# Kernel optimization log

Hardware: AMD Instinct MI355X
Metric: run time of the kernel (lower is better)

Reference implementation:

```python
import jax, jax.numpy as jnp
import numpy as np

B, N, C, H = 16, 577, 384, 6
ONE_DIM = 24
RPD = 2 * ONE_DIM - 1  # 47
NUM_CLS = 1
HEAD_DIM = C // H
SCALE = HEAD_DIM ** -0.5


def _build_rel_pos_index():
    # Faithful to the torch loop: tmp[dy - y + off, dx - x + off] with
    # torch's negative-index wraparound -> modulo RPD.
    off = ONE_DIM // 2
    qy = np.repeat(np.arange(ONE_DIM), ONE_DIM)  # (Np,) y of each query patch
    qx = np.tile(np.arange(ONE_DIM), ONE_DIM)    # (Np,) x of each query patch
    ky, kx = qy, qx                              # key patches use same grid
    ry = (ky[None, :] - qy[:, None] + off) % RPD
    rx = (kx[None, :] - qx[:, None] + off) % RPD
    return jnp.asarray(ry * RPD + rx, dtype=jnp.int32)  # (Np, Np)


def setup_inputs() -> dict:
    key = jax.random.key(0)
    k = jax.random.split(key, 6)
    x = jax.random.normal(k[0], (B, N, C), dtype=jnp.float32)
    qkv_w = jax.random.normal(k[1], (3 * C, C), dtype=jnp.float32) * 0.02
    qkv_b = jnp.zeros((3 * C,), dtype=jnp.float32)
    proj_w = jax.random.normal(k[2], (C, C), dtype=jnp.float32) * 0.02
    proj_b = jnp.zeros((C,), dtype=jnp.float32)
    rel_pos = jax.random.normal(k[3], (H, RPD * RPD), dtype=jnp.float32) * 0.02
    mask = jax.random.randint(k[4], (B, N, N), 0, 2, dtype=jnp.int32)
    return {
        "x": x, "qkv_w": qkv_w, "qkv_b": qkv_b,
        "proj_w": proj_w, "proj_b": proj_b, "rel_pos": rel_pos,
        "rel_pos_index": _build_rel_pos_index(),
        "mask": mask, "patch_attn": 1,
    }


def reference(x, qkv_w, qkv_b, proj_w, proj_b, rel_pos, rel_pos_index, mask, patch_attn):
    # qkv projection: torch Linear -> x @ W^T + b
    qkv = x @ qkv_w.T + qkv_b                               # (B, N, 3C)
    qkv = qkv.reshape(B, N, 3, H, HEAD_DIM).transpose(2, 0, 3, 1, 4)
    q, k, v = qkv[0], qkv[1], qkv[2]                        # (B, H, N, hd)

    attn = jnp.einsum("bhqd,bhkd->bhqk", q, k) * SCALE      # (B, H, N, N)

    if patch_attn:
        # gather per-head relative-position bias for patch tokens
        bias = rel_pos[:, rel_pos_index]                    # (H, Np, Np)
        attn = attn.at[:, :, NUM_CLS:, NUM_CLS:].add(bias)

    neg = jnp.finfo(attn.dtype).min
    attn = jnp.where(mask[:, None, :, :] == 0, neg, attn)   # broadcast over heads

    attn = jax.nn.softmax(attn, axis=-1)
    out = jnp.einsum("bhqk,bhkd->bhqd", attn, v)            # (B, H, N, hd)
    out = out.transpose(0, 2, 1, 3).reshape(B, N, C)
    out = out @ proj_w.T + proj_b
    return out
```

## Files before the change

### kernel.cpp

```cpp
#include <hip/hip_runtime.h>
#include <float.h>
#include <math.h>

#define NB 16
#define NN 577
#define NC 384
#define NH 6
#define ND 64
#define RPD2 2209
#define MTOT 9232
#define MPAD 9344
#define SCALE_ 0.125f
#define NEGBIG -3.0e38f
#define BSTRIDE 580
#define NKPAD 640

typedef __attribute__((ext_vector_type(8))) short bf16x8;
typedef __attribute__((ext_vector_type(4))) float f32x4;
typedef unsigned short u16;

#define MFMA16(a, b, c) __builtin_amdgcn_mfma_f32_16x16x32_bf16(a, b, c, 0, 0, 0)

#define SQA 3932160ull
#define OFF_QH 0ull
#define OFF_QL SQA
#define OFF_KH (2ull * SQA)
#define OFF_KL (3ull * SQA)
#define OFF_VTH (4ull * SQA)
#define OFF_VTL (5ull * SQA)
#define OFF_XH (6ull * SQA)
#define OFF_XL (6ull * SQA + 3588096ull)
#define OFF_WQH (6ull * SQA + 2ull * 3588096ull)
#define OFF_WQL (OFF_WQH + 442368ull)
#define OFF_WPH (OFF_WQL + 442368ull)
#define OFF_WPL (OFF_WPH + 147456ull)
#define OFF_BT  (OFF_WPL + 147456ull)
#define OFF_PM  (OFF_BT + 2007960ull)

static __device__ __forceinline__ u16 f2bf(float f) {
  unsigned u = __float_as_uint(f);
  u += 0x7fff + ((u >> 16) & 1);
  return (u16)(u >> 16);
}
static __device__ __forceinline__ float bf2f(u16 h) {
  return __uint_as_float((unsigned)h << 16);
}
static __device__ __forceinline__ void split2(float v, u16& hi, u16& lo) {
  hi = f2bf(v);
  lo = f2bf(v - bf2f(hi));
}
static __device__ __forceinline__ void gload16(const void* g, void* l) {
  __builtin_amdgcn_global_load_lds(
      (const __attribute__((address_space(1))) void*)g,
      (__attribute__((address_space(3))) void*)l, 16, 0, 0);
}

__global__ __launch_bounds__(256) void split_inputs_k(
    const float* __restrict__ x, const float* __restrict__ wq,
    const float* __restrict__ wp, u16* __restrict__ ws)
{
  const int q = blockIdx.x * 256 + threadIdx.x;
  float4 v = {0.f, 0.f, 0.f, 0.f};
  u16 *dh, *dl;
  if (q < 897024) {
    if (q < 886272) v = ((const float4*)x)[q];
    dh = ws + OFF_XH + 4ull * q;
    dl = ws + OFF_XL + 4ull * q;
  } else if (q < 1007616) {
    int t = q - 897024;
    v = ((const float4*)wq)[t];
    dh = ws + OFF_WQH + 4ull * t;
    dl = ws + OFF_WQL + 4ull * t;
  } else {
    int t = q - 1007616;
    v = ((const float4*)wp)[t];
    dh = ws + OFF_WPH + 4ull * t;
    dl = ws + OFF_WPL + 4ull * t;
  }
  ushort4 hh, ll;
  split2(v.x, hh.x, ll.x);
  split2(v.y, hh.y, ll.y);
  split2(v.z, hh.z, ll.z);
  split2(v.w, hh.w, ll.w);
  *(ushort4*)dh = hh;
  *(ushort4*)dl = ll;
}

__global__ __launch_bounds__(256) void pack_mask_k(const int* __restrict__ mask,
                                                   unsigned* __restrict__ pm)
{
  const int wid = (blockIdx.x * 256 + threadIdx.x) >> 6;
  const int lane = threadIdx.x & 63;
  if (wid >= MTOT) return;
  const int* mr = mask + (size_t)wid * NN;
#pragma unroll
  for (int c = 0; c < 10; ++c) {
    int k = c * 64 + lane;
    int v = (k < NN) ? mr[k] : 0;
    unsigned long long bal = __ballot(v != 0);
    if (lane == 0) pm[wid * 20 + 2 * c] = (unsigned)bal;
    if (lane == 1) pm[wid * 20 + 2 * c + 1] = (unsigned)(bal >> 32);
  }
}

__global__ __launch_bounds__(256) void bias_build_k(
    const float* __restrict__ rel_pos, const int* __restrict__ rel_idx,
    const int* __restrict__ patch, u16* __restrict__ tbl)
{
  const int q = blockIdx.x;
  const int h = blockIdx.y;
  const int pa = *patch;
  u16* row = tbl + ((size_t)h * NN + q) * BSTRIDE;
  for (int kk = threadIdx.x; kk < BSTRIDE; kk += 256) {
    float v = 0.f;
    if (pa && q >= 1 && kk >= 1 && kk < NN)
      v = rel_pos[h * RPD2 + rel_idx[(q - 1) * 576 + (kk - 1)]];
    row[kk] = f2bf(v);
  }
}

__global__ __launch_bounds__(256, 3) void qkv_mfma_k(
    const u16* __restrict__ Xh, const u16* __restrict__ Xl,
    const u16* __restrict__ Wh, const u16* __restrict__ Wl,
    const float* __restrict__ bias, u16* __restrict__ ws)
{
  __shared__ u16 Ash[4096], Asl[4096];
  __shared__ u16 Bsh[4096], Bsl[4096];

  const int tid = threadIdx.x;
  const int w = tid >> 6, l = tid & 63, lq = l & 15, lg = l >> 4;
  const int wm = (w >> 1) * 64, wn = (w & 1) * 64;
  const int mb = blockIdx.x * 128;
  const int rb = blockIdx.y * 128;
  const int r0 = rb + wn;
  const int soff = (l >> 2) * 384 + (l & 3) * 8;

  f32x4 acc[4][4];
#pragma unroll
  for (int nt = 0; nt < 4; ++nt) {
    float bv = bias[r0 + 16 * nt + lq];
#pragma unroll
    for (int mt = 0; mt < 4; ++mt) acc[mt][nt] = (f32x4){bv, bv, bv, bv};
  }

  for (int k0 = 0; k0 < 384; k0 += 32) {
    __syncthreads();
#pragma unroll
    for (int j = 0; j < 2; ++j) {
      const int tr = 32 * w + 16 * j;
      const size_t ga = (size_t)(mb + tr) * 384 + k0 + soff;
      const size_t gb = (size_t)(rb + tr) * 384 + k0 + soff;
      gload16(&Xh[ga], &Ash[tr * 32]);
      gload16(&Xl[ga], &Asl[tr * 32]);
      gload16(&Wh[gb], &Bsh[tr * 32]);
      gload16(&Wl[gb], &Bsl[tr * 32]);
    }
    __syncthreads();

    bf16x8 bhf[4], blf[4];
#pragma unroll
    for (int nt = 0; nt < 4; ++nt) {
      bhf[nt] = *(const bf16x8*)&Bsh[(wn + 16 * nt + lq) * 32 + 8 * lg];
      blf[nt] = *(const bf16x8*)&Bsl[(wn + 16 * nt + lq) * 32 + 8 * lg];
    }
#pragma unroll
    for (int mt = 0; mt < 4; ++mt) {
      bf16x8 ah = *(const bf16x8*)&Ash[(wm + 16 * mt + lq) * 32 + 8 * lg];
      bf16x8 al = *(const bf16x8*)&Asl[(wm + 16 * mt + lq) * 32 + 8 * lg];
#pragma unroll
      for (int nt = 0; nt < 4; ++nt) {
        acc[mt][nt] = MFMA16(ah, bhf[nt], acc[mt][nt]);
        acc[mt][nt] = MFMA16(ah, blf[nt], acc[mt][nt]);
        acc[mt][nt] = MFMA16(al, bhf[nt], acc[mt][nt]);
      }
    }
  }

  const int comp = rb / 384;
  const int h = ((rb % 384) + wn) >> 6;
#pragma unroll
  for (int mt = 0; mt < 4; ++mt)
#pragma unroll
    for (int r = 0; r < 4; ++r) {
      int m = mb + wm + 16 * mt + 4 * lg + r;
      if (m >= MTOT) continue;
      int bb = m / NN, nn = m - bb * NN;
      int bh = bb * NH + h;
#pragma unroll
      for (int nt = 0; nt < 4; ++nt) {
        int d = 16 * nt + lq;
        float v = acc[mt][nt][r];
        u16 hi, lo;
        if (comp == 0) {
          v *= SCALE_;
          split2(v, hi, lo);
          size_t a = ((size_t)bh * NKPAD + nn) * 64 + d;
          ws[OFF_QH + a] = hi;
          ws[OFF_QL + a] = lo;
        } else if (comp == 1) {
          split2(v, hi, lo);
          size_t a = ((size_t)bh * NKPAD + nn) * 64 + d;
          ws[OFF_KH + a] = hi;
          ws[OFF_KL + a] = lo;
        } else {
          split2(v, hi, lo);
          size_t a = ((size_t)bh * 64 + d) * NKPAD + nn;
          ws[OFF_VTH + a] = hi;
          ws[OFF_VTL + a] = lo;
        }
      }
    }
}

__global__ __launch_bounds__(256, 2) void attn_k(
    const u16* __restrict__ Qh, const u16* __restrict__ Ql,
    const u16* __restrict__ Kh, const u16* __restrict__ Kl,
    const u16* __restrict__ Vth, const u16* __restrict__ Vtl,
    const u16* __restrict__ btbl, const unsigned* __restrict__ pm,
    u16* __restrict__ Oh, u16* __restrict__ Ol)
{
  __shared__ u16 Kth[2][4096], Ktl[2][4096];
  __shared__ u16 Vsh[2][4096], Vsl[2][4096];
  __shared__ u16 Ph[4][1024];

  const int tid = threadIdx.x;
  const int w = tid >> 6, l = tid & 63, lq = l & 15, lg = l >> 4;
  const int q0 = blockIdx.x * 64;
  const int h = blockIdx.y, b = blockIdx.z;
  const int bh = b * NH + h;
  const int qrow = q0 + 16 * w + lq;
  const int swz = (lq & 7) << 3;
  const int ln8 = l >> 3, lc8 = l & 7;
  const int koff = ln8 * 64 + ((lc8 ^ ln8) << 3);
  const int voff = ln8 * NKPAD + ((lc8 ^ ln8) << 3);

#define STAGE(ch, bf)                                                        \
  {                                                                          \
    const int kb_ = (ch) * 64;                                               \
    const size_t kgb = ((size_t)bh * NKPAD + kb_ + 16 * w) * 64 + koff;      \
    const size_t vgb = ((size_t)bh * 64 + 16 * w) * NKPAD + kb_ + voff;      \
    gload16(&Kh[kgb],              &Kth[bf][(16 * w) * 64]);                 \
    gload16(&Kh[kgb + 512],        &Kth[bf][(16 * w + 8) * 64]);             \
    gload16(&Kl[kgb],              &Ktl[bf][(16 * w) * 64]);                 \
    gload16(&Kl[kgb + 512],        &Ktl[bf][(16 * w + 8) * 64]);             \
    gload16(&Vth[vgb],             &Vsh[bf][(16 * w) * 64]);                 \
    gload16(&Vth[vgb + 8 * NKPAD], &Vsh[bf][(16 * w + 8) * 64]);             \
    gload16(&Vtl[vgb],             &Vsl[bf][(16 * w) * 64]);                 \
    gload16(&Vtl[vgb + 8 * NKPAD], &Vsl[bf][(16 * w + 8) * 64]);             \
  }

  STAGE(0, 0);

  const size_t qbase = ((size_t)bh * NKPAD + qrow) * 64 + 8 * lg;
  bf16x8 qbh[2], qbl[2];
  qbh[0] = *(const bf16x8*)&Qh[qbase];
  qbh[1] = *(const bf16x8*)&Qh[qbase + 32];
  qbl[0] = *(const bf16x8*)&Ql[qbase];
  qbl[1] = *(const bf16x8*)&Ql[qbase + 32];

  const bool qv = qrow < NN;
  const int gqc = qv ? qrow : NN - 1;
  const unsigned* pmrow = pm + ((size_t)b * NN + gqc) * 20;
  const size_t brow = ((size_t)h * NN + gqc) * BSTRIDE;

  float m_reg = NEGBIG, l_reg = 0.f;
  f32x4 accO[4] = {};

  for (int ch = 0; ch < 10; ++ch) {
    const int kb = ch * 64;
    const int bf = ch & 1;
    __syncthreads();
    if (ch < 9) STAGE(ch + 1, bf ^ 1);

    unsigned long long m64 = (unsigned long long)pmrow[2 * ch] |
                             ((unsigned long long)pmrow[2 * ch + 1] << 32);
    f32x4 cinit[4];
#pragma unroll
    for (int t = 0; t < 4; ++t) {
      cinit[t] = (f32x4){0.f, 0.f, 0.f, 0.f};
      int kkb = kb + 16 * t + 4 * lg;
      if (qv && kkb <= 576) {
        ushort4 b4 = *(const ushort4*)&btbl[brow + kkb];
        cinit[t][0] = bf2f(b4.x); cinit[t][1] = bf2f(b4.y);
        cinit[t][2] = bf2f(b4.z); cinit[t][3] = bf2f(b4.w);
      }
    }

    float sv[4][4];
#pragma unroll
    for (int t = 0; t < 4; ++t) {
      f32x4 acc = cinit[t];
      const int ar = (16 * t + lq) * 64;
#pragma unroll
      for (int ks = 0; ks < 2; ++ks) {
        const int c = (8 * lg + 32 * ks) ^ swz;
        bf16x8 ah = *(const bf16x8*)&Kth[bf][ar + c];
        bf16x8 al = *(const bf16x8*)&Ktl[bf][ar + c];
        acc = MFMA16(ah, qbh[ks], acc);
        acc = MFMA16(ah, qbl[ks], acc);
        acc = MFMA16(al, qbh[ks], acc);
      }
      sv[t][0] = acc[0]; sv[t][1] = acc[1];
      sv[t][2] = acc[2]; sv[t][3] = acc[3];
    }

    float cmax = NEGBIG;
#pragma unroll
    for (int t = 0; t < 4; ++t)
#pragma unroll
      for (int r = 0; r < 4; ++r) {
        int kl = 16 * t + 4 * lg + r;
        float s = ((m64 >> kl) & 1ull) ? sv[t][r] : NEGBIG;
        sv[t][r] = s;
        cmax = fmaxf(cmax, s);
      }
    cmax = fmaxf(cmax, __shfl_xor(cmax, 16));
    cmax = fmaxf(cmax, __shfl_xor(cmax, 32));
    float m_new = fmaxf(m_reg, cmax);
    float fx = __expf(m_reg - m_new);
    float csum = 0.f;
    float ev[4][4];
#pragma unroll
    for (int t = 0; t < 4; ++t)
#pragma unroll
      for (int r = 0; r < 4; ++r) {
        float e = __expf(sv[t][r] - m_new);
        ev[t][r] = e;
        csum += e;
      }
    csum += __shfl_xor(csum, 16);
    csum += __shfl_xor(csum, 32);
    l_reg = l_reg * fx + csum;
    m_reg = m_new;

#pragma unroll
    for (int t = 0; t < 4; ++t) {
      ushort4 ph;
      ph.x = f2bf(ev[t][0]);
      ph.y = f2bf(ev[t][1]);
      ph.z = f2bf(ev[t][2]);
      ph.w = f2bf(ev[t][3]);
      int c = (16 * t + 4 * lg) ^ swz;
      *(ushort4*)&Ph[w][lq * 64 + c] = ph;
    }

    float fxr[4];
#pragma unroll
    for (int r = 0; r < 4; ++r) fxr[r] = __shfl(fx, 4 * lg + r);
#pragma unroll
    for (int t = 0; t < 4; ++t) {
      accO[t][0] *= fxr[0]; accO[t][1] *= fxr[1];
      accO[t][2] *= fxr[2]; accO[t][3] *= fxr[3];
    }

    bf16x8 pah[2];
#pragma unroll
    for (int ks = 0; ks < 2; ++ks) {
      int c = (8 * lg + 32 * ks) ^ swz;
      pah[ks] = *(const bf16x8*)&Ph[w][lq * 64 + c];
    }

#pragma unroll
    for (int t = 0; t < 4; ++t) {
      const int vr = (16 * t + lq) * 64;
#pragma unroll
      for (int ks = 0; ks < 2; ++ks) {
        const int c = (8 * lg + 32 * ks) ^ swz;
        bf16x8 vh = *(const bf16x8*)&Vsh[bf][vr + c];
        bf16x8 vl = *(const bf16x8*)&Vsl[bf][vr + c];
        accO[t] = MFMA16(pah[ks], vh, accO[t]);
        accO[t] = MFMA16(pah[ks], vl, accO[t]);
      }
    }
  }

  float il = 1.f / l_reg;
  float ilr[4];
#pragma unroll
  for (int r = 0; r < 4; ++r) ilr[r] = __shfl(il, 4 * lg + r);
#pragma unroll
  for (int t = 0; t < 4; ++t)
#pragma unroll
    for (int r = 0; r < 4; ++r) {
      int gq2 = q0 + 16 * w + 4 * lg + r;
      if (gq2 < NN) {
        float v = accO[t][r] * ilr[r];
        u16 hi, lo;
        split2(v, hi, lo);
        size_t a = ((size_t)b * NN + gq2) * NC + h * 64 + 16 * t + lq;
        Oh[a] = hi;
        Ol[a] = lo;
      }
    }
#undef STAGE
}

__global__ __launch_bounds__(256, 3) void proj_mfma_k(
    const u16* __restrict__ Ah, const u16* __restrict__ Al,
    const u16* __restrict__ Wh, const u16* __restrict__ Wl,
    const float* __restrict__ bias, float* __restrict__ out)
{
  __shared__ u16 Ash[4096], Asl[4096];
  __shared__ u16 Bsh[4096], Bsl[4096];

  const int tid = threadIdx.x;
  const int w = tid >> 6, l = tid & 63, lq = l & 15, lg = l >> 4;
  const int wm = (w >> 1) * 64, wn = (w & 1) * 64;
  const int mb = blockIdx.x * 128;
  const int rb = blockIdx.y * 128;
  const int r0 = rb + wn;
  const int soff = (l >> 2) * 384 + (l & 3) * 8;

  f32x4 acc[4][4];
#pragma unroll
  for (int nt = 0; nt < 4; ++nt) {
    float bv = bias[r0 + 16 * nt + lq];
#pragma unroll
    for (int mt = 0; mt < 4; ++mt) acc[mt][nt] = (f32x4){bv, bv, bv, bv};
  }

  for (int k0 = 0; k0 < 384; k0 += 32) {
    __syncthreads();
#pragma unroll
    for (int j = 0; j < 2; ++j) {
      const int tr = 32 * w + 16 * j;
      const size_t ga = (size_t)(mb + tr) * 384 + k0 + soff;
      const size_t gb = (size_t)(rb + tr) * 384 + k0 + soff;
      gload16(&Ah[ga], &Ash[tr * 32]);
      gload16(&Al[ga], &Asl[tr * 32]);
      gload16(&Wh[gb], &Bsh[tr * 32]);
      gload16(&Wl[gb], &Bsl[tr * 32]);
    }
    __syncthreads();

    bf16x8 bhf[4], blf[4];
#pragma unroll
    for (int nt = 0; nt < 4; ++nt) {
      bhf[nt] = *(const bf16x8*)&Bsh[(wn + 16 * nt + lq) * 32 + 8 * lg];
      blf[nt] = *(const bf16x8*)&Bsl[(wn + 16 * nt + lq) * 32 + 8 * lg];
    }
#pragma unroll
    for (int mt = 0; mt < 4; ++mt) {
      bf16x8 ah = *(const bf16x8*)&Ash[(wm + 16 * mt + lq) * 32 + 8 * lg];
      bf16x8 al = *(const bf16x8*)&Asl[(wm + 16 * mt + lq) * 32 + 8 * lg];
#pragma unroll
      for (int nt = 0; nt < 4; ++nt) {
        acc[mt][nt] = MFMA16(ah, bhf[nt], acc[mt][nt]);
        acc[mt][nt] = MFMA16(ah, blf[nt], acc[mt][nt]);
        acc[mt][nt] = MFMA16(al, bhf[nt], acc[mt][nt]);
      }
    }
  }

#pragma unroll
  for (int mt = 0; mt < 4; ++mt)
#pragma unroll
    for (int r = 0; r < 4; ++r) {
      int m = mb + wm + 16 * mt + 4 * lg + r;
      if (m >= MTOT) continue;
#pragma unroll
      for (int nt = 0; nt < 4; ++nt)
        out[(size_t)m * NC + r0 + 16 * nt + lq] = acc[mt][nt][r];
    }
}

extern "C" void kernel_launch(void* const* d_in, const int* in_sizes, int n_in,
                              void* d_out, int out_size, void* d_ws, size_t ws_size,
                              hipStream_t stream) {
  const float* x       = (const float*)d_in[0];
  const float* qkv_w   = (const float*)d_in[1];
  const float* qkv_b   = (const float*)d_in[2];
  const float* proj_w  = (const float*)d_in[3];
  const float* proj_b  = (const float*)d_in[4];
  const float* rel_pos = (const float*)d_in[5];
  const int*   rel_idx = (const int*)d_in[6];
  const int*   mask    = (const int*)d_in[7];
  const int*   patch   = (const int*)d_in[8];
  float* out = (float*)d_out;
  u16* W16 = (u16*)d_ws;

  unsigned* pmp = (unsigned*)(W16 + OFF_PM);
  u16* btblp = W16 + OFF_BT;

  split_inputs_k<<<4080, 256, 0, stream>>>(x, qkv_w, proj_w, W16);
  pack_mask_k<<<2308, 256, 0, stream>>>(mask, pmp);
  bias_build_k<<<dim3(NN, NH), 256, 0, stream>>>(rel_pos, rel_idx, patch, btblp);
  qkv_mfma_k<<<dim3(73, 9), 256, 0, stream>>>(
      W16 + OFF_XH, W16 + OFF_XL, W16 + OFF_WQH, W16 + OFF_WQL, qkv_b, W16);
  attn_k<<<dim3(10, NH, NB), 256, 0, stream>>>(
      W16 + OFF_QH, W16 + OFF_QL, W16 + OFF_KH, W16 + OFF_KL,
      W16 + OFF_VTH, W16 + OFF_VTL, btblp, pmp,
      W16 + OFF_XH, W16 + OFF_XL);
  proj_mfma_k<<<dim3(73, 3), 256, 0, stream>>>(
      W16 + OFF_XH, W16 + OFF_XL, W16 + OFF_WPH, W16 + OFF_WPL, proj_b, out);
}
```

Measured before the change: 171.2 us.

## Double query tile per attention block; stream weights directly and double-buffer A in GEMMs

The attention kernel now handles 128 query rows per block, with each wave owning two 16-row query tiles. Every staged K/V chunk is therefore reused for twice as many queries, and the grid shrinks from 10 to 5 query blocks per (batch, head). The QKV and projection GEMMs no longer stage weight tiles in shared memory; they read the B fragments straight from global memory and double-buffer the activation tile, which removes one barrier per k-step. In exchange, attention register pressure roughly doubles and the grid gets smaller, and the direct weight loads depend on cache hits.

```diff
diff --git a/kernel.cpp b/kernel.cpp
--- a/kernel.cpp
+++ b/kernel.cpp
@@ -124,8 +124,7 @@
     const u16* __restrict__ Wh, const u16* __restrict__ Wl,
     const float* __restrict__ bias, u16* __restrict__ ws)
 {
-  __shared__ u16 Ash[4096], Asl[4096];
-  __shared__ u16 Bsh[4096], Bsl[4096];
+  __shared__ u16 Ash[2][4096], Asl[2][4096];
 
   const int tid = threadIdx.x;
   const int w = tid >> 6, l = tid & 63, lq = l & 15, lg = l >> 4;
@@ -135,6 +134,19 @@
   const int r0 = rb + wn;
   const int soff = (l >> 2) * 384 + (l & 3) * 8;
 
+#define STAGE_A(k0_, bf_)                                                    \
+  {                                                                          \
+    _Pragma("unroll")                                                        \
+    for (int j = 0; j < 2; ++j) {                                            \
+      const int tr = 32 * w + 16 * j;                                        \
+      const size_t ga = (size_t)(mb + tr) * 384 + (k0_) + soff;              \
+      gload16(&Xh[ga], &Ash[bf_][tr * 32]);                                  \
+      gload16(&Xl[ga], &Asl[bf_][tr * 32]);                                  \
+    }                                                                        \
+  }
+
+  STAGE_A(0, 0);
+
   f32x4 acc[4][4];
 #pragma unroll
   for (int nt = 0; nt < 4; ++nt) {
@@ -143,30 +155,22 @@
     for (int mt = 0; mt < 4; ++mt) acc[mt][nt] = (f32x4){bv, bv, bv, bv};
   }
 
+  const size_t brow = (size_t)(r0 + lq) * 384 + 8 * lg;
   for (int k0 = 0; k0 < 384; k0 += 32) {
+    const int bf = (k0 >> 5) & 1;
     __syncthreads();
-#pragma unroll
-    for (int j = 0; j < 2; ++j) {
-      const int tr = 32 * w + 16 * j;
-      const size_t ga = (size_t)(mb + tr) * 384 + k0 + soff;
-      const size_t gb = (size_t)(rb + tr) * 384 + k0 + soff;
-      gload16(&Xh[ga], &Ash[tr * 32]);
-      gload16(&Xl[ga], &Asl[tr * 32]);
-      gload16(&Wh[gb], &Bsh[tr * 32]);
-      gload16(&Wl[gb], &Bsl[tr * 32]);
-    }
-    __syncthreads();
+    if (k0 < 352) STAGE_A(k0 + 32, bf ^ 1);
 
     bf16x8 bhf[4], blf[4];
 #pragma unroll
     for (int nt = 0; nt < 4; ++nt) {
-      bhf[nt] = *(const bf16x8*)&Bsh[(wn + 16 * nt + lq) * 32 + 8 * lg];
-      blf[nt] = *(const bf16x8*)&Bsl[(wn + 16 * nt + lq) * 32 + 8 * lg];
+      bhf[nt] = *(const bf16x8*)&Wh[brow + (size_t)(16 * nt) * 384 + k0];
+      blf[nt] = *(const bf16x8*)&Wl[brow + (size_t)(16 * nt) * 384 + k0];
     }
 #pragma unroll
     for (int mt = 0; mt < 4; ++mt) {
-      bf16x8 ah = *(const bf16x8*)&Ash[(wm + 16 * mt + lq) * 32 + 8 * lg];
-      bf16x8 al = *(const bf16x8*)&Asl[(wm + 16 * mt + lq) * 32 + 8 * lg];
+      bf16x8 ah = *(const bf16x8*)&Ash[bf][(wm + 16 * mt + lq) * 32 + 8 * lg];
+      bf16x8 al = *(const bf16x8*)&Asl[bf][(wm + 16 * mt + lq) * 32 + 8 * lg];
 #pragma unroll
       for (int nt = 0; nt < 4; ++nt) {
         acc[mt][nt] = MFMA16(ah, bhf[nt], acc[mt][nt]);
@@ -175,6 +179,7 @@
       }
     }
   }
+#undef STAGE_A
 
   const int comp = rb / 384;
   const int h = ((rb % 384) + wn) >> 6;
@@ -221,14 +226,15 @@
 {
   __shared__ u16 Kth[2][4096], Ktl[2][4096];
   __shared__ u16 Vsh[2][4096], Vsl[2][4096];
-  __shared__ u16 Ph[4][1024];
+  __shared__ u16 Ph[4][2048];
 
   const int tid = threadIdx.x;
   const int w = tid >> 6, l = tid & 63, lq = l & 15, lg = l >> 4;
-  const int q0 = blockIdx.x * 64;
+  const int q0 = blockIdx.x * 128;
   const int h = blockIdx.y, b = blockIdx.z;
   const int bh = b * NH + h;
-  const int qrow = q0 + 16 * w + lq;
+  const int qr0 = q0 + 32 * w + lq;
+  const int qr1 = qr0 + 16;
   const int swz = (lq & 7) << 3;
   const int ln8 = l >> 3, lc8 = l & 7;
   const int koff = ln8 * 64 + ((lc8 ^ ln8) << 3);
@@ -251,20 +257,29 @@
 
   STAGE(0, 0);
 
-  const size_t qbase = ((size_t)bh * NKPAD + qrow) * 64 + 8 * lg;
-  bf16x8 qbh[2], qbl[2];
-  qbh[0] = *(const bf16x8*)&Qh[qbase];
-  qbh[1] = *(const bf16x8*)&Qh[qbase + 32];
-  qbl[0] = *(const bf16x8*)&Ql[qbase];
-  qbl[1] = *(const bf16x8*)&Ql[qbase + 32];
-
-  const bool qv = qrow < NN;
-  const int gqc = qv ? qrow : NN - 1;
-  const unsigned* pmrow = pm + ((size_t)b * NN + gqc) * 20;
-  const size_t brow = ((size_t)h * NN + gqc) * BSTRIDE;
-
-  float m_reg = NEGBIG, l_reg = 0.f;
-  f32x4 accO[4] = {};
+  const size_t qb0 = ((size_t)bh * NKPAD + qr0) * 64 + 8 * lg;
+  const size_t qb1 = ((size_t)bh * NKPAD + qr1) * 64 + 8 * lg;
+  bf16x8 q0h[2], q0l[2], q1h[2], q1l[2];
+  q0h[0] = *(const bf16x8*)&Qh[qb0];
+  q0h[1] = *(const bf16x8*)&Qh[qb0 + 32];
+  q0l[0] = *(const bf16x8*)&Ql[qb0];
+  q0l[1] = *(const bf16x8*)&Ql[qb0 + 32];
+  q1h[0] = *(const bf16x8*)&Qh[qb1];
+  q1h[1] = *(const bf16x8*)&Qh[qb1 + 32];
+  q1l[0] = *(const bf16x8*)&Ql[qb1];
+  q1l[1] = *(const bf16x8*)&Ql[qb1 + 32];
+
+  const int gq0 = (qr0 < NN) ? qr0 : NN - 1;
+  const int gq1 = (qr1 < NN) ? qr1 : NN - 1;
+  const bool qv0 = qr0 < NN, qv1 = qr1 < NN;
+  const unsigned* pmrow0 = pm + ((size_t)b * NN + gq0) * 20;
+  const unsigned* pmrow1 = pm + ((size_t)b * NN + gq1) * 20;
+  const size_t brow0 = ((size_t)h * NN + gq0) * BSTRIDE;
+  const size_t brow1 = ((size_t)h * NN + gq1) * BSTRIDE;
+
+  float m_reg0 = NEGBIG, l_reg0 = 0.f;
+  float m_reg1 = NEGBIG, l_reg1 = 0.f;
+  f32x4 accO0[4] = {}, accO1[4] = {};
 
   for (int ch = 0; ch < 10; ++ch) {
     const int kb = ch * 64;
@@ -272,92 +287,138 @@
     __syncthreads();
     if (ch < 9) STAGE(ch + 1, bf ^ 1);
 
-    unsigned long long m64 = (unsigned long long)pmrow[2 * ch] |
-                             ((unsigned long long)pmrow[2 * ch + 1] << 32);
-    f32x4 cinit[4];
+    unsigned long long m64_0 = (unsigned long long)pmrow0[2 * ch] |
+                               ((unsigned long long)pmrow0[2 * ch + 1] << 32);
+    unsigned long long m64_1 = (unsigned long long)pmrow1[2 * ch] |
+                               ((unsigned long long)pmrow1[2 * ch + 1] << 32);
+    f32x4 ci0[4], ci1[4];
 #pragma unroll
     for (int t = 0; t < 4; ++t) {
-      cinit[t] = (f32x4){0.f, 0.f, 0.f, 0.f};
+      ci0[t] = (f32x4){0.f, 0.f, 0.f, 0.f};
+      ci1[t] = (f32x4){0.f, 0.f, 0.f, 0.f};
       int kkb = kb + 16 * t + 4 * lg;
-      if (qv && kkb <= 576) {
-        ushort4 b4 = *(const ushort4*)&btbl[brow + kkb];
-        cinit[t][0] = bf2f(b4.x); cinit[t][1] = bf2f(b4.y);
-        cinit[t][2] = bf2f(b4.z); cinit[t][3] = bf2f(b4.w);
-      }
-    }
-
-    float sv[4][4];
+      if (kkb <= 576) {
+        if (qv0) {
+          ushort4 b4 = *(const ushort4*)&btbl[brow0 + kkb];
+          ci0[t][0] = bf2f(b4.x); ci0[t][1] = bf2f(b4.y);
+          ci0[t][2] = bf2f(b4.z); ci0[t][3] = bf2f(b4.w);
+        }
+        if (qv1) {
+          ushort4 b4 = *(const ushort4*)&btbl[brow1 + kkb];
+          ci1[t][0] = bf2f(b4.x); ci1[t][1] = bf2f(b4.y);
+          ci1[t][2] = bf2f(b4.z); ci1[t][3] = bf2f(b4.w);
+        }
+      }
+    }
+
+    float sv0[4][4], sv1[4][4];
 #pragma unroll
     for (int t = 0; t < 4; ++t) {
-      f32x4 acc = cinit[t];
+      f32x4 a0 = ci0[t], a1 = ci1[t];
       const int ar = (16 * t + lq) * 64;
 #pragma unroll
       for (int ks = 0; ks < 2; ++ks) {
         const int c = (8 * lg + 32 * ks) ^ swz;
         bf16x8 ah = *(const bf16x8*)&Kth[bf][ar + c];
         bf16x8 al = *(const bf16x8*)&Ktl[bf][ar + c];
-        acc = MFMA16(ah, qbh[ks], acc);
-        acc = MFMA16(ah, qbl[ks], acc);
-        acc = MFMA16(al, qbh[ks], acc);
-      }
-      sv[t][0] = acc[0]; sv[t][1] = acc[1];
-      sv[t][2] = acc[2]; sv[t][3] = acc[3];
-    }
-
-    float cmax = NEGBIG;
-#pragma unroll
-    for (int t = 0; t < 4; ++t)
-#pragma unroll
-      for (int r = 0; r < 4; ++r) {
-        int kl = 16 * t + 4 * lg + r;
-        float s = ((m64 >> kl) & 1ull) ? sv[t][r] : NEGBIG;
-        sv[t][r] = s;
-        cmax = fmaxf(cmax, s);
-      }
-    cmax = fmaxf(cmax, __shfl_xor(cmax, 16));
-    cmax = fmaxf(cmax, __shfl_xor(cmax, 32));
-    float m_new = fmaxf(m_reg, cmax);
-    float fx = __expf(m_reg - m_new);
-    float csum = 0.f;
-    float ev[4][4];
-#pragma unroll
-    for (int t = 0; t < 4; ++t)
-#pragma unroll
-      for (int r = 0; r < 4; ++r) {
-        float e = __expf(sv[t][r] - m_new);
-        ev[t][r] = e;
-        csum += e;
-      }
-    csum += __shfl_xor(csum, 16);
-    csum += __shfl_xor(csum, 32);
-    l_reg = l_reg * fx + csum;
-    m_reg = m_new;
-
-#pragma unroll
-    for (int t = 0; t < 4; ++t) {
-      ushort4 ph;
-      ph.x = f2bf(ev[t][0]);
-      ph.y = f2bf(ev[t][1]);
-      ph.z = f2bf(ev[t][2]);
-      ph.w = f2bf(ev[t][3]);
-      int c = (16 * t + 4 * lg) ^ swz;
-      *(ushort4*)&Ph[w][lq * 64 + c] = ph;
-    }
-
-    float fxr[4];
-#pragma unroll
-    for (int r = 0; r < 4; ++r) fxr[r] = __shfl(fx, 4 * lg + r);
-#pragma unroll
-    for (int t = 0; t < 4; ++t) {
-      accO[t][0] *= fxr[0]; accO[t][1] *= fxr[1];
-      accO[t][2] *= fxr[2]; accO[t][3] *= fxr[3];
-    }
-
-    bf16x8 pah[2];
+        a0 = MFMA16(ah, q0h[ks], a0);
+        a0 = MFMA16(ah, q0l[ks], a0);
+        a0 = MFMA16(al, q0h[ks], a0);
+        a1 = MFMA16(ah, q1h[ks], a1);
+        a1 = MFMA16(ah, q1l[ks], a1);
+        a1 = MFMA16(al, q1h[ks], a1);
+      }
+#pragma unroll
+      for (int r = 0; r < 4; ++r) { sv0[t][r] = a0[r]; sv1[t][r] = a1[r]; }
+    }
+
+    {
+      float cmax = NEGBIG;
+#pragma unroll
+      for (int t = 0; t < 4; ++t)
+#pragma unroll
+        for (int r = 0; r < 4; ++r) {
+          int kl = 16 * t + 4 * lg + r;
+          float s = ((m64_0 >> kl) & 1ull) ? sv0[t][r] : NEGBIG;
+          sv0[t][r] = s;
+          cmax = fmaxf(cmax, s);
+        }
+      cmax = fmaxf(cmax, __shfl_xor(cmax, 16));
+      cmax = fmaxf(cmax, __shfl_xor(cmax, 32));
+      float m_new = fmaxf(m_reg0, cmax);
+      float fx = __expf(m_reg0 - m_new);
+      float csum = 0.f;
+#pragma unroll
+      for (int t = 0; t < 4; ++t) {
+        float e0 = __expf(sv0[t][0] - m_new);
+        float e1 = __expf(sv0[t][1] - m_new);
+        float e2 = __expf(sv0[t][2] - m_new);
+        float e3 = __expf(sv0[t][3] - m_new);
+        csum += e0 + e1 + e2 + e3;
+        ushort4 ph;
+        ph.x = f2bf(e0); ph.y = f2bf(e1); ph.z = f2bf(e2); ph.w = f2bf(e3);
+        *(ushort4*)&Ph[w][lq * 64 + ((16 * t + 4 * lg) ^ swz)] = ph;
+      }
+      csum += __shfl_xor(csum, 16);
+      csum += __shfl_xor(csum, 32);
+      l_reg0 = l_reg0 * fx + csum;
+      m_reg0 = m_new;
+      float fxr[4];
+#pragma unroll
+      for (int r = 0; r < 4; ++r) fxr[r] = __shfl(fx, 4 * lg + r);
+#pragma unroll
+      for (int t = 0; t < 4; ++t) {
+        accO0[t][0] *= fxr[0]; accO0[t][1] *= fxr[1];
+        accO0[t][2] *= fxr[2]; accO0[t][3] *= fxr[3];
+      }
+    }
+    {
+      float cmax = NEGBIG;
+#pragma unroll
+      for (int t = 0; t < 4; ++t)
+#pragma unroll
+        for (int r = 0; r < 4; ++r) {
+          int kl = 16 * t + 4 * lg + r;
+          float s = ((m64_1 >> kl) & 1ull) ? sv1[t][r] : NEGBIG;
+          sv1[t][r] = s;
+          cmax = fmaxf(cmax, s);
+        }
+      cmax = fmaxf(cmax, __shfl_xor(cmax, 16));
+      cmax = fmaxf(cmax, __shfl_xor(cmax, 32));
+      float m_new = fmaxf(m_reg1, cmax);
+      float fx = __expf(m_reg1 - m_new);
+      float csum = 0.f;
+#pragma unroll
+      for (int t = 0; t < 4; ++t) {
+        float e0 = __expf(sv1[t][0] - m_new);
+        float e1 = __expf(sv1[t][1] - m_new);
+        float e2 = __expf(sv1[t][2] - m_new);
+        float e3 = __expf(sv1[t][3] - m_new);
+        csum += e0 + e1 + e2 + e3;
+        ushort4 ph;
+        ph.x = f2bf(e0); ph.y = f2bf(e1); ph.z = f2bf(e2); ph.w = f2bf(e3);
+        *(ushort4*)&Ph[w][(16 + lq) * 64 + ((16 * t + 4 * lg) ^ swz)] = ph;
+      }
+      csum += __shfl_xor(csum, 16);
+      csum += __shfl_xor(csum, 32);
+      l_reg1 = l_reg1 * fx + csum;
+      m_reg1 = m_new;
+      float fxr[4];
+#pragma unroll
+      for (int r = 0; r < 4; ++r) fxr[r] = __shfl(fx, 4 * lg + r);
+#pragma unroll
+      for (int t = 0; t < 4; ++t) {
+        accO1[t][0] *= fxr[0]; accO1[t][1] *= fxr[1];
+        accO1[t][2] *= fxr[2]; accO1[t][3] *= fxr[3];
+      }
+    }
+
+    bf16x8 pa0[2], pa1[2];
 #pragma unroll
     for (int ks = 0; ks < 2; ++ks) {
       int c = (8 * lg + 32 * ks) ^ swz;
-      pah[ks] = *(const bf16x8*)&Ph[w][lq * 64 + c];
+      pa0[ks] = *(const bf16x8*)&Ph[w][lq * 64 + c];
+      pa1[ks] = *(const bf16x8*)&Ph[w][(16 + lq) * 64 + c];
     }
 
 #pragma unroll
@@ -368,31 +429,46 @@
         const int c = (8 * lg + 32 * ks) ^ swz;
         bf16x8 vh = *(const bf16x8*)&Vsh[bf][vr + c];
         bf16x8 vl = *(const bf16x8*)&Vsl[bf][vr + c];
-        accO[t] = MFMA16(pah[ks], vh, accO[t]);
-        accO[t] = MFMA16(pah[ks], vl, accO[t]);
-      }
-    }
-  }
-
-  float il = 1.f / l_reg;
-  float ilr[4];
-#pragma unroll
-  for (int r = 0; r < 4; ++r) ilr[r] = __shfl(il, 4 * lg + r);
+        accO0[t] = MFMA16(pa0[ks], vh, accO0[t]);
+        accO0[t] = MFMA16(pa0[ks], vl, accO0[t]);
+        accO1[t] = MFMA16(pa1[ks], vh, accO1[t]);
+        accO1[t] = MFMA16(pa1[ks], vl, accO1[t]);
+      }
+    }
+  }
+#undef STAGE
+
+  float il0 = 1.f / l_reg0;
+  float il1 = 1.f / l_reg1;
+  float ilr0[4], ilr1[4];
+#pragma unroll
+  for (int r = 0; r < 4; ++r) {
+    ilr0[r] = __shfl(il0, 4 * lg + r);
+    ilr1[r] = __shfl(il1, 4 * lg + r);
+  }
 #pragma unroll
   for (int t = 0; t < 4; ++t)
 #pragma unroll
     for (int r = 0; r < 4; ++r) {
-      int gq2 = q0 + 16 * w + 4 * lg + r;
-      if (gq2 < NN) {
-        float v = accO[t][r] * ilr[r];
+      int g0 = q0 + 32 * w + 4 * lg + r;
+      if (g0 < NN) {
+        float v = accO0[t][r] * ilr0[r];
         u16 hi, lo;
         split2(v, hi, lo);
-        size_t a = ((size_t)b * NN + gq2) * NC + h * 64 + 16 * t + lq;
+        size_t a = ((size_t)b * NN + g0) * NC + h * 64 + 16 * t + lq;
         Oh[a] = hi;
         Ol[a] = lo;
       }
-    }
-#undef STAGE
+      int g1 = g0 + 16;
+      if (g1 < NN) {
+        float v = accO1[t][r] * ilr1[r];
+        u16 hi, lo;
+        split2(v, hi, lo);
+        size_t a = ((size_t)b * NN + g1) * NC + h * 64 + 16 * t + lq;
+        Oh[a] = hi;
+        Ol[a] = lo;
+      }
+    }
 }
 
 __global__ __launch_bounds__(256, 3) void proj_mfma_k(
@@ -400,8 +476,7 @@
     const u16* __restrict__ Wh, const u16* __restrict__ Wl,
     const float* __restrict__ bias, float* __restrict__ out)
 {
-  __shared__ u16 Ash[4096], Asl[4096];
-  __shared__ u16 Bsh[4096], Bsl[4096];
+  __shared__ u16 Ash[2][4096], Asl[2][4096];
 
   const int tid = threadIdx.x;
   const int w = tid >> 6, l = tid & 63, lq = l & 15, lg = l >> 4;
@@ -411,6 +486,19 @@
   const int r0 = rb + wn;
   const int soff = (l >> 2) * 384 + (l & 3) * 8;
 
+#define STAGE_A(k0_, bf_)                                                    \
+  {                                                                          \
+    _Pragma("unroll")                                                        \
+    for (int j = 0; j < 2; ++j) {                                            \
+      const int tr = 32 * w + 16 * j;                                        \
+      const size_t ga = (size_t)(mb + tr) * 384 + (k0_) + soff;              \
+      gload16(&Ah[ga], &Ash[bf_][tr * 32]);                                  \
+      gload16(&Al[ga], &Asl[bf_][tr * 32]);                                  \
+    }                                                                        \
+  }
+
+  STAGE_A(0, 0);
+
   f32x4 acc[4][4];
 #pragma unroll
   for (int nt = 0; nt < 4; ++nt) {
@@ -419,30 +507,22 @@
     for (int mt = 0; mt < 4; ++mt) acc[mt][nt] = (f32x4){bv, bv, bv, bv};
   }
 
+  const size_t brow = (size_t)(r0 + lq) * 384 + 8 * lg;
   for (int k0 = 0; k0 < 384; k0 += 32) {
+    const int bf = (k0 >> 5) & 1;
     __syncthreads();
-#pragma unroll
-    for (int j = 0; j < 2; ++j) {
-      const int tr = 32 * w + 16 * j;
-      const size_t ga = (size_t)(mb + tr) * 384 + k0 + soff;
-      const size_t gb = (size_t)(rb + tr) * 384 + k0 + soff;
-      gload16(&Ah[ga], &Ash[tr * 32]);
-      gload16(&Al[ga], &Asl[tr * 32]);
-      gload16(&Wh[gb], &Bsh[tr * 32]);
-      gload16(&Wl[gb], &Bsl[tr * 32]);
-    }
-    __syncthreads();
+    if (k0 < 352) STAGE_A(k0 + 32, bf ^ 1);
 
     bf16x8 bhf[4], blf[4];
 #pragma unroll
     for (int nt = 0; nt < 4; ++nt) {
-      bhf[nt] = *(const bf16x8*)&Bsh[(wn + 16 * nt + lq) * 32 + 8 * lg];
-      blf[nt] = *(const bf16x8*)&Bsl[(wn + 16 * nt + lq) * 32 + 8 * lg];
+      bhf[nt] = *(const bf16x8*)&Wh[brow + (size_t)(16 * nt) * 384 + k0];
+      blf[nt] = *(const bf16x8*)&Wl[brow + (size_t)(16 * nt) * 384 + k0];
     }
 #pragma unroll
     for (int mt = 0; mt < 4; ++mt) {
-      bf16x8 ah = *(const bf16x8*)&Ash[(wm + 16 * mt + lq) * 32 + 8 * lg];
-      bf16x8 al = *(const bf16x8*)&Asl[(wm + 16 * mt + lq) * 32 + 8 * lg];
+      bf16x8 ah = *(const bf16x8*)&Ash[bf][(wm + 16 * mt + lq) * 32 + 8 * lg];
+      bf16x8 al = *(const bf16x8*)&Asl[bf][(wm + 16 * mt + lq) * 32 + 8 * lg];
 #pragma unroll
       for (int nt = 0; nt < 4; ++nt) {
         acc[mt][nt] = MFMA16(ah, bhf[nt], acc[mt][nt]);
@@ -451,6 +531,7 @@
       }
     }
   }
+#undef STAGE_A
 
 #pragma unroll
   for (int mt = 0; mt < 4; ++mt)
@@ -487,7 +568,7 @@
   bias_build_k<<<dim3(NN, NH), 256, 0, stream>>>(rel_pos, rel_idx, patch, btblp);
   qkv_mfma_k<<<dim3(73, 9), 256, 0, stream>>>(
       W16 + OFF_XH, W16 + OFF_XL, W16 + OFF_WQH, W16 + OFF_WQL, qkv_b, W16);
-  attn_k<<<dim3(10, NH, NB), 256, 0, stream>>>(
+  attn_k<<<dim3(5, NH, NB), 256, 0, stream>>>(
       W16 + OFF_QH, W16 + OFF_QL, W16 + OFF_KH, W16 + OFF_KL,
       W16 + OFF_VTH, W16 + OFF_VTL, btblp, pmp,
       W16 + OFF_XH, W16 + OFF_XL);
```

After: 179.4 us. 4.8% more time.
